# Kernel tuning notes

Hardware: AMD Instinct MI355X
Metric: run time of the kernel (lower is better)

The kernel has to match this reference:

```python
import jax, jax.numpy as jnp
import numpy as np

N_HEADS = 12


def setup_inputs() -> dict:
    key = jax.random.key(0)
    ks = jax.random.split(key, 4)
    B, T, C = 1, 4096, 768
    x = jax.random.normal(ks[0], (B, T, C), dtype=jnp.float32)
    w_qkv = jax.random.normal(ks[1], (C, 3 * C), dtype=jnp.float32) * (C ** -0.5)
    b_qkv = jnp.zeros((3 * C,), dtype=jnp.float32)
    w_proj = jax.random.normal(ks[2], (C, C), dtype=jnp.float32) * (C ** -0.5)
    b_proj = jnp.zeros((C,), dtype=jnp.float32)
    return {"x": x, "w_qkv": w_qkv, "b_qkv": b_qkv, "w_proj": w_proj, "b_proj": b_proj}


def reference(x, w_qkv, b_qkv, w_proj, b_proj):
    B, T, C = x.shape
    H = N_HEADS
    hd = C // H
    qkv = x @ w_qkv + b_qkv                      # [B,T,3C]
    q, k, v = jnp.split(qkv, 3, axis=-1)
    # [B,H,T,hd]
    q = q.reshape(B, T, H, hd).transpose(0, 2, 1, 3)
    k = k.reshape(B, T, H, hd).transpose(0, 2, 1, 3)
    v = v.reshape(B, T, H, hd).transpose(0, 2, 1, 3)
    scale = 1.0 / jnp.sqrt(jnp.float32(hd))
    attn = jnp.einsum('bhqd,bhkd->bhqk', q, k) * scale  # [B,H,T,T]
    causal = jnp.tril(jnp.ones((T, T), dtype=bool))
    attn = jnp.where(causal, attn, jnp.float32(-jnp.inf))
    attn = jax.nn.softmax(attn, axis=-1)
    out = jnp.einsum('bhqk,bhkd->bhqd', attn, v)        # [B,H,T,hd]
    out = out.transpose(0, 2, 1, 3).reshape(B, T, C)
    return out @ w_proj + b_proj
```

## Files before the change

### kernel.cpp

```cpp
#include <hip/hip_runtime.h>
#include <hip/hip_bf16.h>


#define T_SEQ 4096
#define C_DIM 768
#define C3    2304
#define NH    12
#define HD    64

typedef __attribute__((ext_vector_type(8))) short bf16x8;
typedef __attribute__((ext_vector_type(4))) float f32x4;

__device__ inline unsigned short f2bf(float f) {
  union { float f; unsigned u; } v; v.f = f;
  unsigned r = v.u + 0x7fff + ((v.u >> 16) & 1);
  return (unsigned short)(r >> 16);
}
__device__ inline unsigned short f2bf_trunc(float f) {
  union { float f; unsigned u; } v; v.f = f;
  return (unsigned short)(v.u >> 16);
}

__device__ inline void store_out(float v, float* p) { *p = v; }
__device__ inline void store_out(float v, unsigned short* p) { *p = f2bf(v); }

__device__ inline void gl2lds16(const void* g, void* l) {
  __builtin_amdgcn_global_load_lds(
      (const __attribute__((address_space(1))) unsigned int*)g,
      (__attribute__((address_space(3))) unsigned int*)l, 16, 0, 0);
}

#if __has_builtin(__builtin_amdgcn_exp2f)
#define EXP2F(x) __builtin_amdgcn_exp2f(x)
#else
#define EXP2F(x) exp2f(x)
#endif

#define NB_CONV  (T_SEQ * C_DIM / 2048)
#define NB_TQKV  ((C3 / 32) * (C_DIM / 32))
#define NB_TPROJ ((C_DIM / 32) * (C_DIM / 32))

__global__ __launch_bounds__(256) void prep_fused(
    const float* __restrict__ x, const float* __restrict__ w_qkv,
    const float* __restrict__ w_proj, unsigned short* __restrict__ xb,
    unsigned short* __restrict__ wqkvT, unsigned short* __restrict__ wprojT) {
  __shared__ float t[32][33];
  const int b = blockIdx.x;
  const int tid = threadIdx.x;

  if (b < NB_CONV) {
    int i = (b * 256 + tid) * 8;
    float4 v0 = *(const float4*)(x + i);
    float4 v1 = *(const float4*)(x + i + 4);
    unsigned short o[8] = {f2bf(v0.x), f2bf(v0.y), f2bf(v0.z), f2bf(v0.w),
                           f2bf(v1.x), f2bf(v1.y), f2bf(v1.z), f2bf(v1.w)};
    *(uint4*)(xb + i) = *(uint4*)o;
    return;
  }
  const float* in;
  unsigned short* outT;
  int R, Cc, bi;
  if (b < NB_CONV + NB_TQKV) {
    in = w_qkv; outT = wqkvT; R = C_DIM; Cc = C3; bi = b - NB_CONV;
  } else {
    in = w_proj; outT = wprojT; R = C_DIM; Cc = C_DIM; bi = b - NB_CONV - NB_TQKV;
  }
  const int tx = tid & 31, ty = tid >> 5;
  const int c0 = (bi % (Cc / 32)) * 32, r0 = (bi / (Cc / 32)) * 32;
#pragma unroll
  for (int i = 0; i < 4; ++i) {
    int r = ty + i * 8;
    t[r][tx] = in[(size_t)(r0 + r) * Cc + c0 + tx];
  }
  __syncthreads();
#pragma unroll
  for (int i = 0; i < 4; ++i) {
    int c = ty + i * 8;
    outT[(size_t)(c0 + c) * R + r0 + tx] = f2bf(t[tx][c]);
  }
}

__global__ __launch_bounds__(256) void transpose_v_perm(
    const unsigned short* __restrict__ qkv, unsigned short* __restrict__ vTp) {
  __shared__ unsigned short t[32][33];
  const int tx = threadIdx.x & 31, ty = threadIdx.x >> 5;
  const int c0 = blockIdx.x * 32;
  const int r0 = blockIdx.y * 32;
#pragma unroll
  for (int i = 0; i < 4; ++i) {
    int r = ty + i * 8;
    t[r][tx] = qkv[(size_t)(r0 + r) * C3 + 2 * C_DIM + c0 + tx];
  }
  __syncthreads();
  const int pos = (tx < 16) ? (8 * (tx >> 2) + (tx & 3))
                            : (8 * ((tx - 16) >> 2) + 4 + ((tx - 16) & 3));
#pragma unroll
  for (int i = 0; i < 4; ++i) {
    int c = ty + i * 8;
    vTp[(size_t)(c0 + c) * T_SEQ + r0 + pos] = t[tx][c];
  }
}

template <typename OutT>
__global__ __launch_bounds__(256) void gemm_bt_mfma(
    const unsigned short* __restrict__ A, const unsigned short* __restrict__ Bt,
    const float* __restrict__ bias, OutT* __restrict__ C,
    int M, int N, int K) {
  __shared__ unsigned short As[128 * 32];
  __shared__ unsigned short Bs[128 * 32];
  const int tid = threadIdx.x;
  const int wave = tid >> 6, lane = tid & 63;
  const int lo = lane & 15, g8 = lane >> 4;
  const int wm = wave >> 1, wn = wave & 1;
  const int bm = blockIdx.y * 128, bn = blockIdx.x * 128;
  const int lrow = lane >> 2;
  const int lcol = (lane & 3) * 8;

  f32x4 acc[4][4];
#pragma unroll
  for (int mt = 0; mt < 4; ++mt)
#pragma unroll
    for (int nt = 0; nt < 4; ++nt) acc[mt][nt] = (f32x4){0.f, 0.f, 0.f, 0.f};

  const unsigned short* Abase = A + (size_t)bm * K;
  const unsigned short* Bbase = Bt + (size_t)bn * K;

  for (int k0 = 0; k0 < K; k0 += 32) {
    __syncthreads();
#pragma unroll
    for (int c = 0; c < 2; ++c) {
      const int r = wave * 32 + c * 16;
      gl2lds16(Abase + (size_t)(r + lrow) * K + k0 + lcol, As + r * 32 + lane * 8);
      gl2lds16(Bbase + (size_t)(r + lrow) * K + k0 + lcol, Bs + r * 32 + lane * 8);
    }
    __syncthreads();

    bf16x8 a[4], b[4];
#pragma unroll
    for (int mt = 0; mt < 4; ++mt)
      a[mt] = *(const bf16x8*)(As + (wm * 64 + mt * 16 + lo) * 32 + g8 * 8);
#pragma unroll
    for (int nt = 0; nt < 4; ++nt)
      b[nt] = *(const bf16x8*)(Bs + (wn * 64 + nt * 16 + lo) * 32 + g8 * 8);
#pragma unroll
    for (int mt = 0; mt < 4; ++mt)
#pragma unroll
      for (int nt = 0; nt < 4; ++nt)
        acc[mt][nt] = __builtin_amdgcn_mfma_f32_16x16x32_bf16(a[mt], b[nt], acc[mt][nt], 0, 0, 0);
  }

#pragma unroll
  for (int nt = 0; nt < 4; ++nt) {
    const int n = bn + wn * 64 + nt * 16 + lo;
    const float bv = bias[n];
#pragma unroll
    for (int mt = 0; mt < 4; ++mt)
#pragma unroll
      for (int r = 0; r < 4; ++r) {
        const int m = bm + wm * 64 + mt * 16 + g8 * 4 + r;
        store_out(acc[mt][nt][r] + bv, &C[(size_t)m * N + n]);
      }
  }
}

__global__ __launch_bounds__(256) void flash_attn_mfma7(
    const unsigned short* __restrict__ qkv,
    const unsigned short* __restrict__ vTp,
    unsigned short* __restrict__ out) {
  __shared__ unsigned short Ks[2][64 * 64];
  __shared__ unsigned short Vs[2][64 * 64];

  const int qt = 63 - blockIdx.x / NH;
  const int h = blockIdx.x % NH;
  const int q0 = qt * 64;
  const int tid = threadIdx.x;
  const int w = tid >> 6;
  const int lane = tid & 63;
  const int lo = lane & 15;
  const int g = lane >> 4;
  const int lo7 = lo & 7;
  const float qscale = 0.125f * 1.44269504f;

  const unsigned short* Kg = qkv + C_DIM + h * HD;
  const unsigned short* Vg = vTp + (size_t)(h * HD) * T_SEQ;

  const int drow = tid >> 3;
  const int dslot = (tid & 7) * 8;
  const int dsrc = ((tid & 7) ^ (drow & 7)) * 8;

  bf16x8 qb[2];
#pragma unroll
  for (int dh = 0; dh < 2; ++dh)
    qb[dh] = *(const bf16x8*)(
        qkv + (size_t)(q0 + w * 16 + lo) * C3 + h * HD + dh * 32 + g * 8);

#pragma unroll
  for (int p = 0; p < 2; ++p) {
    const int r = p * 32 + drow;
    gl2lds16(Kg + (size_t)r * C3 + dsrc, Ks[0] + r * 64 + dslot);
    gl2lds16(Vg + (size_t)r * T_SEQ + dsrc, Vs[0] + r * 64 + dslot);
  }
  __syncthreads();

  float m_i = -1e30f, l_i = 0.f;
  f32x4 o_acc[4];
#pragma unroll
  for (int dt = 0; dt < 4; ++dt) o_acc[dt] = (f32x4){0.f, 0.f, 0.f, 0.f};

  for (int t = 0; t <= qt; ++t) {
    const int cur = t & 1;
    if (t < qt) {
      const int k0n = (t + 1) * 64;
#pragma unroll
      for (int p = 0; p < 2; ++p) {
        const int r = p * 32 + drow;
        gl2lds16(Kg + (size_t)(k0n + r) * C3 + dsrc, Ks[cur ^ 1] + r * 64 + dslot);
        gl2lds16(Vg + (size_t)r * T_SEQ + k0n + dsrc, Vs[cur ^ 1] + r * 64 + dslot);
      }
    }

    f32x4 st[4];
#pragma unroll
    for (int mt = 0; mt < 4; ++mt) st[mt] = (f32x4){0.f, 0.f, 0.f, 0.f};
#pragma unroll
    for (int mt = 0; mt < 4; ++mt)
#pragma unroll
      for (int dh = 0; dh < 2; ++dh) {
        bf16x8 a = *(const bf16x8*)(
            Ks[cur] + (mt * 16 + lo) * 64 + (((dh * 4 + g) ^ lo7) * 8));
        st[mt] = __builtin_amdgcn_mfma_f32_16x16x32_bf16(a, qb[dh], st[mt], 0, 0, 0);
      }

    if (t == qt) {
      const int qloc = w * 16 + lo;
#pragma unroll
      for (int mt = 0; mt < 4; ++mt)
#pragma unroll
        for (int r = 0; r < 4; ++r)
          if (mt * 16 + g * 4 + r > qloc) st[mt][r] = -1e30f;
    }
    float mx = -1e30f;
#pragma unroll
    for (int mt = 0; mt < 4; ++mt)
#pragma unroll
      for (int r = 0; r < 4; ++r) mx = fmaxf(mx, st[mt][r]);
    mx = fmaxf(mx, __shfl_xor(mx, 16));
    mx = fmaxf(mx, __shfl_xor(mx, 32));
    const float mnew = fmaxf(m_i, mx);
    const float alpha = EXP2F((m_i - mnew) * qscale);
    m_i = mnew;
    const float ms = mnew * qscale;
    float e[4][4];
    float lsum = 0.f;
#pragma unroll
    for (int mt = 0; mt < 4; ++mt)
#pragma unroll
      for (int r = 0; r < 4; ++r) {
        float v = EXP2F(__builtin_fmaf(st[mt][r], qscale, -ms));
        e[mt][r] = v;
        lsum += v;
      }
    lsum += __shfl_xor(lsum, 16);
    lsum += __shfl_xor(lsum, 32);
    bf16x8 pt[2];
#pragma unroll
    for (int kh = 0; kh < 2; ++kh) {
#pragma unroll
      for (int j = 0; j < 4; ++j) {
        pt[kh][j] = (short)f2bf_trunc(e[kh * 2][j]);
        pt[kh][4 + j] = (short)f2bf_trunc(e[kh * 2 + 1][j]);
      }
    }
    if (__any(alpha != 1.0f)) {
      l_i *= alpha;
#pragma unroll
      for (int dt = 0; dt < 4; ++dt)
#pragma unroll
        for (int r = 0; r < 4; ++r) o_acc[dt][r] *= alpha;
    }
    l_i += lsum;

#pragma unroll
    for (int dt = 0; dt < 4; ++dt)
#pragma unroll
      for (int kh = 0; kh < 2; ++kh) {
        bf16x8 av = *(const bf16x8*)(
            Vs[cur] + (dt * 16 + lo) * 64 + (((kh * 4 + g) ^ lo7) * 8));
        o_acc[dt] = __builtin_amdgcn_mfma_f32_16x16x32_bf16(av, pt[kh], o_acc[dt], 0, 0, 0);
      }

    __syncthreads();
  }

  const float inv = 1.0f / l_i;
#pragma unroll
  for (int dt = 0; dt < 4; ++dt) {
    const int chunk = (dt * 2 + (g >> 1)) ^ lo7;
#pragma unroll
    for (int r = 0; r < 4; ++r)
      Ks[0][(w * 16 + lo) * 64 + chunk * 8 + (g & 1) * 4 + r] =
          f2bf(o_acc[dt][r] * inv);
  }
#pragma unroll
  for (int i = 0; i < 2; ++i) {
    const int row = w * 16 + i * 8 + (lane >> 3);
    bf16x8 val = *(const bf16x8*)(Ks[0] + row * 64 + (((lane & 7) ^ (row & 7)) * 8));
    *(bf16x8*)(out + (size_t)(q0 + row) * C_DIM + h * HD + (lane & 7) * 8) = val;
  }
}

extern "C" void kernel_launch(void* const* d_in, const int* in_sizes, int n_in,
                              void* d_out, int out_size, void* d_ws, size_t ws_size,
                              hipStream_t stream) {
  const float* x      = (const float*)d_in[0];
  const float* w_qkv  = (const float*)d_in[1];
  const float* b_qkv  = (const float*)d_in[2];
  const float* w_proj = (const float*)d_in[3];
  const float* b_proj = (const float*)d_in[4];
  float* out = (float*)d_out;

  unsigned short* xb     = (unsigned short*)d_ws;
  unsigned short* wqkvT  = xb + (size_t)T_SEQ * C_DIM;
  unsigned short* wprojT = wqkvT + (size_t)C3 * C_DIM;
  unsigned short* qkv    = wprojT + (size_t)C_DIM * C_DIM;
  unsigned short* vTp    = qkv + (size_t)T_SEQ * C3;
  unsigned short* attnb  = vTp + (size_t)C_DIM * T_SEQ;

  prep_fused<<<NB_CONV + NB_TQKV + NB_TPROJ, 256, 0, stream>>>(
      x, w_qkv, w_proj, xb, wqkvT, wprojT);

  gemm_bt_mfma<unsigned short><<<dim3(C3 / 128, T_SEQ / 128), 256, 0, stream>>>(
      xb, wqkvT, b_qkv, qkv, T_SEQ, C3, C_DIM);

  transpose_v_perm<<<dim3(C_DIM / 32, T_SEQ / 32), 256, 0, stream>>>(qkv, vTp);

  flash_attn_mfma7<<<T_SEQ / 64 * NH, 256, 0, stream>>>(qkv, vTp, attnb);

  gemm_bt_mfma<float><<<dim3(C_DIM / 128, T_SEQ / 128), 256, 0, stream>>>(
      attnb, wprojT, b_proj, out, T_SEQ, C_DIM, C_DIM);
}
```

Before: 203.3 us.

## Use 128-query attention blocks with 8 waves sharing K/V tiles

Doubles the query tile per attention block from 64 to 128 rows using 512 threads, so each K/V tile staged in LDS serves twice as many queries, and each thread now loads one row per tile. Causal masking becomes per-wave, based on global positions. This cuts K/V global-to-LDS traffic and loop overhead per query, but halves the block count and adds partially masked wasted work on diagonal tiles for the lower waves. The output staging reuses the whole contiguous K buffer region.

```diff
diff --git a/kernel.cpp b/kernel.cpp
--- a/kernel.cpp
+++ b/kernel.cpp
@@ -163,16 +163,17 @@
   }
 }
 
-__global__ __launch_bounds__(256) void flash_attn_mfma7(
+__global__ __launch_bounds__(512) void flash_attn_mfma8(
     const unsigned short* __restrict__ qkv,
     const unsigned short* __restrict__ vTp,
     unsigned short* __restrict__ out) {
   __shared__ unsigned short Ks[2][64 * 64];
   __shared__ unsigned short Vs[2][64 * 64];
 
-  const int qt = 63 - blockIdx.x / NH;
+  const int qi = 31 - blockIdx.x / NH;
   const int h = blockIdx.x % NH;
-  const int q0 = qt * 64;
+  const int q0 = qi * 128;
+  const int tmax = 2 * qi + 1;
   const int tid = threadIdx.x;
   const int w = tid >> 6;
   const int lane = tid & 63;
@@ -194,12 +195,8 @@
     qb[dh] = *(const bf16x8*)(
         qkv + (size_t)(q0 + w * 16 + lo) * C3 + h * HD + dh * 32 + g * 8);
 
-#pragma unroll
-  for (int p = 0; p < 2; ++p) {
-    const int r = p * 32 + drow;
-    gl2lds16(Kg + (size_t)r * C3 + dsrc, Ks[0] + r * 64 + dslot);
-    gl2lds16(Vg + (size_t)r * T_SEQ + dsrc, Vs[0] + r * 64 + dslot);
-  }
+  gl2lds16(Kg + (size_t)drow * C3 + dsrc, Ks[0] + drow * 64 + dslot);
+  gl2lds16(Vg + (size_t)drow * T_SEQ + dsrc, Vs[0] + drow * 64 + dslot);
   __syncthreads();
 
   float m_i = -1e30f, l_i = 0.f;
@@ -207,16 +204,12 @@
 #pragma unroll
   for (int dt = 0; dt < 4; ++dt) o_acc[dt] = (f32x4){0.f, 0.f, 0.f, 0.f};
 
-  for (int t = 0; t <= qt; ++t) {
+  for (int t = 0; t <= tmax; ++t) {
     const int cur = t & 1;
-    if (t < qt) {
+    if (t < tmax) {
       const int k0n = (t + 1) * 64;
-#pragma unroll
-      for (int p = 0; p < 2; ++p) {
-        const int r = p * 32 + drow;
-        gl2lds16(Kg + (size_t)(k0n + r) * C3 + dsrc, Ks[cur ^ 1] + r * 64 + dslot);
-        gl2lds16(Vg + (size_t)r * T_SEQ + k0n + dsrc, Vs[cur ^ 1] + r * 64 + dslot);
-      }
+      gl2lds16(Kg + (size_t)(k0n + drow) * C3 + dsrc, Ks[cur ^ 1] + drow * 64 + dslot);
+      gl2lds16(Vg + (size_t)drow * T_SEQ + k0n + dsrc, Vs[cur ^ 1] + drow * 64 + dslot);
     }
 
     f32x4 st[4];
@@ -231,14 +224,15 @@
         st[mt] = __builtin_amdgcn_mfma_f32_16x16x32_bf16(a, qb[dh], st[mt], 0, 0, 0);
       }
 
-    if (t == qt) {
-      const int qloc = w * 16 + lo;
+    if (t * 64 + 63 > q0 + w * 16) {
+      const int qglob = q0 + w * 16 + lo;
 #pragma unroll
       for (int mt = 0; mt < 4; ++mt)
 #pragma unroll
         for (int r = 0; r < 4; ++r)
-          if (mt * 16 + g * 4 + r > qloc) st[mt][r] = -1e30f;
-    }
+          if (t * 64 + mt * 16 + g * 4 + r > qglob) st[mt][r] = -1e30f;
+    }
+
     float mx = -1e30f;
 #pragma unroll
     for (int mt = 0; mt < 4; ++mt)
@@ -293,18 +287,19 @@
   }
 
   const float inv = 1.0f / l_i;
+  unsigned short* Es = Ks[0];
 #pragma unroll
   for (int dt = 0; dt < 4; ++dt) {
     const int chunk = (dt * 2 + (g >> 1)) ^ lo7;
 #pragma unroll
     for (int r = 0; r < 4; ++r)
-      Ks[0][(w * 16 + lo) * 64 + chunk * 8 + (g & 1) * 4 + r] =
+      Es[(w * 16 + lo) * 64 + chunk * 8 + (g & 1) * 4 + r] =
           f2bf(o_acc[dt][r] * inv);
   }
 #pragma unroll
   for (int i = 0; i < 2; ++i) {
     const int row = w * 16 + i * 8 + (lane >> 3);
-    bf16x8 val = *(const bf16x8*)(Ks[0] + row * 64 + (((lane & 7) ^ (row & 7)) * 8));
+    bf16x8 val = *(const bf16x8*)(Es + row * 64 + (((lane & 7) ^ (row & 7)) * 8));
     *(bf16x8*)(out + (size_t)(q0 + row) * C_DIM + h * HD + (lane & 7) * 8) = val;
   }
 }
@@ -334,7 +329,7 @@
 
   transpose_v_perm<<<dim3(C_DIM / 32, T_SEQ / 32), 256, 0, stream>>>(qkv, vTp);
 
-  flash_attn_mfma7<<<T_SEQ / 64 * NH, 256, 0, stream>>>(qkv, vTp, attnb);
+  flash_attn_mfma8<<<T_SEQ / 128 * NH, 512, 0, stream>>>(qkv, vTp, attnb);
 
   gemm_bt_mfma<float><<<dim3(C_DIM / 128, T_SEQ / 128), 256, 0, stream>>>(
       attnb, wprojT, b_proj, out, T_SEQ, C_DIM, C_DIM);
```

Result: slower. 208.7 us (+2.7%).
